# Optimization experiments

Hardware: AMD Instinct MI355X
Metric: run time of the kernel (lower is better)

Reference implementation:

```python
import jax, jax.numpy as jnp
import numpy as np

T, B = 200, 4096
CONTEXT_FRAMES = 6


def _lstm_cell(x, h, c, wih, whh, bih, bhh):
    # PyTorch LSTM gate order: i, f, g, o
    g = x @ wih.T + bih + h @ whh.T + bhh
    i, f, gg, o = jnp.split(g, 4, axis=-1)
    c2 = jax.nn.sigmoid(f) * c + jax.nn.sigmoid(i) * jnp.tanh(gg)
    h2 = jax.nn.sigmoid(o) * jnp.tanh(c2)
    return h2, c2


def _ff(x, w1, b1, w2, b2):
    return jax.nn.relu(jax.nn.relu(x @ w1.T + b1) @ w2.T + b2)


def setup_inputs() -> dict:
    key = jax.random.key(0)
    ks = iter(jax.random.split(key, 48))

    def p(shape, scale=0.1):
        return (jax.random.normal(next(ks), shape) * scale).astype(jnp.float32)

    inp = {
        'tactiles': p((T, B, 48), 1.0),
        'actions': p((T, B, 3), 1.0),
        'context': p((T, B, 48), 1.0),
    }
    # LSTM params: (4H, in), (4H, H), (4H,), (4H,)
    for name, din, h in [('l1', 48, 48), ('l2', 96, 96), ('l3', 144, 144), ('l4', 48, 48)]:
        inp[name + '_wih'] = p((4 * h, din))
        inp[name + '_whh'] = p((4 * h, h))
        inp[name + '_bih'] = p((4 * h,))
        inp[name + '_bhh'] = p((4 * h,))
    # Feedforward params
    for name, din, hid, dout in [('f1', 6, 48, 48), ('f2', 144, 144, 96), ('f3', 96, 96, 48)]:
        inp[name + '_w1'] = p((hid, din))
        inp[name + '_b1'] = p((hid,))
        inp[name + '_w2'] = p((dout, hid))
        inp[name + '_b2'] = p((dout,))
    # Hidden-state inits (original uses torch.rand -> uniform[0,1))
    for name, h in [('1', 48), ('2', 96), ('3', 144), ('4', 48)]:
        inp['h0_' + name] = jax.random.uniform(next(ks), (B, h), dtype=jnp.float32)
        inp['c0_' + name] = jax.random.uniform(next(ks), (B, h), dtype=jnp.float32)
    return inp


def reference(tactiles, actions, context,
              l1_wih, l1_whh, l1_bih, l1_bhh,
              l2_wih, l2_whh, l2_bih, l2_bhh,
              l3_wih, l3_whh, l3_bih, l3_bhh,
              l4_wih, l4_whh, l4_bih, l4_bhh,
              f1_w1, f1_b1, f1_w2, f1_b2,
              f2_w1, f2_b1, f2_w2, f2_b2,
              f3_w1, f3_b1, f3_w2, f3_b2,
              h0_1, c0_1, h0_2, c0_2, h0_3, c0_3, h0_4, c0_4):
    state = actions[0]  # [B, 3], fixed across time

    def step(carry, inp):
        h1, c1, h2, c2, h3, c3, h4, c4, out6 = carry
        tac, act, ctx, t = inp
        x1 = jnp.where(t > CONTEXT_FRAMES - 1, out6, tac)  # [B, 48]
        h1, c1 = _lstm_cell(x1, h1, c1, l1_wih, l1_whh, l1_bih, l1_bhh)
        x2 = jnp.concatenate([ctx, h1], axis=1)  # [B, 96]
        h2, c2 = _lstm_cell(x2, h2, c2, l2_wih, l2_whh, l2_bih, l2_bhh)
        sa = jnp.concatenate([state, act], axis=1)  # [B, 6]
        sa_out = _ff(sa, f1_w1, f1_b1, f1_w2, f1_b2)  # [B, 48]
        x3 = jnp.concatenate([sa_out, h2], axis=1)  # [B, 144]
        h3, c3 = _lstm_cell(x3, h3, c3, l3_wih, l3_whh, l3_bih, l3_bhh)
        out4 = _ff(h3, f2_w1, f2_b1, f2_w2, f2_b2)  # [B, 96]
        out5 = _ff(out4, f3_w1, f3_b1, f3_w2, f3_b2)  # [B, 48]
        h4, c4 = _lstm_cell(out5, h4, c4, l4_wih, l4_whh, l4_bih, l4_bhh)
        return (h1, c1, h2, c2, h3, c3, h4, c4, h4), h4

    carry0 = (h0_1, c0_1, h0_2, c0_2, h0_3, c0_3, h0_4, c0_4, jnp.zeros_like(h0_1))
    ts = jnp.arange(tactiles.shape[0])
    _, outs = jax.lax.scan(step, carry0, (tactiles, actions, context, ts))
    return outs  # [T, B, 48]
```

## Files before the change

kernel.cpp:

```cpp
#include <hip/hip_runtime.h>
#include <math.h>


#define NT 256
#define MROWS 16
#define TSTEPS 200
#define BATCH 4096
#define XS 18
#define GS 17
#define GS8 9

#define L1W   0
#define L1B   18432
#define L2W   18624
#define L2B   92352
#define L3W   92736
#define L3B   258624
#define L4W   259200
#define L4B   277632
#define F1AW  277824
#define F1AB  278208
#define F1BW  278256
#define F1BB  280560
#define F2AW  280608
#define F2AB  301344
#define F2BW  301488
#define F2BB  315312
#define F3AW  315408
#define F3AB  324624
#define F3BW  324720
#define F3BB  329328

#define P_SAT  0
#define P_F1H  144
#define P_GB   0
#define P_F2H  0
#define P_O4T  2592
#define P_F3H  4320
#define P_OUT5 0
#define P_L4G  864
#define POOLSZ 6528

__device__ __forceinline__ float sigf(float x) { return 1.0f / (1.0f + __expf(-x)); }

__global__ void prep_lstm(const float* __restrict__ wih, const float* __restrict__ whh,
                          const float* __restrict__ bih, const float* __restrict__ bhh,
                          float* __restrict__ W, float* __restrict__ bias,
                          int Din, int H) {
    int K = Din + H;
    int N = 4 * H;
    int total = N * K;
    for (int idx = blockIdx.x * blockDim.x + threadIdx.x; idx < total + N;
         idx += gridDim.x * blockDim.x) {
        if (idx < total) {
            int c = idx / K;
            int k = idx - c * K;
            W[idx] = (k < Din) ? wih[c * Din + k] : whh[c * H + (k - Din)];
        } else {
            int c = idx - total;
            bias[c] = bih[c] + bhh[c];
        }
    }
}

__global__ void prep_ff(const float* __restrict__ w, const float* __restrict__ b,
                        float* __restrict__ W, float* __restrict__ bias,
                        int K, int Kpad, int N) {
    int total = N * Kpad;
    for (int idx = blockIdx.x * blockDim.x + threadIdx.x; idx < total + N;
         idx += gridDim.x * blockDim.x) {
        if (idx < total) {
            int c = idx / Kpad;
            int k = idx - c * Kpad;
            W[idx] = (k < K) ? w[c * K + k] : 0.0f;
        } else {
            int c = idx - total;
            bias[c] = b[c];
        }
    }
}

template <int TC, int ROWS, bool RELU>
__device__ __forceinline__ void mm(
    const float* __restrict__ w0, const float* __restrict__ w1,
    const float* __restrict__ w2,
    float b0, float b1, float b2,
    const float* __restrict__ x0, int K0,
    const float* __restrict__ x1, int K1,
    const float* __restrict__ x2, int K2,
    int rbase,
    float* __restrict__ g0, float* __restrict__ g1, float* __restrict__ g2) {
    float a0[ROWS], a1[ROWS], a2[ROWS];
#pragma unroll
    for (int r = 0; r < ROWS; ++r) { a0[r] = 0.f; a1[r] = 0.f; a2[r] = 0.f; }
    int ko = 0;
#pragma unroll
    for (int s = 0; s < 3; ++s) {
        const float* xb = (s == 0) ? x0 : (s == 1) ? x1 : x2;
        int K = (s == 0) ? K0 : (s == 1) ? K1 : K2;
        if (K > 0) {
            const float* xp = xb + rbase;
#pragma unroll 2
            for (int k = 0; k < K; k += 4) {
                float4 wv0 = *(const float4*)(w0 + ko + k);
                float4 wv1 = (TC > 1) ? *(const float4*)(w1 + ko + k) : wv0;
                float4 wv2 = (TC > 2) ? *(const float4*)(w2 + ko + k) : wv0;
                const float* f0 = (const float*)&wv0;
                const float* f1p = (const float*)&wv1;
                const float* f2p = (const float*)&wv2;
#pragma unroll
                for (int q = 0; q < 4; ++q) {
                    const float* xq = xp + (k + q) * XS;
#pragma unroll
                    for (int rr = 0; rr < ROWS; rr += 2) {
                        float2 xv = *(const float2*)(xq + rr);
                        a0[rr]     = fmaf(xv.x, f0[q], a0[rr]);
                        a0[rr + 1] = fmaf(xv.y, f0[q], a0[rr + 1]);
                        if (TC > 1) {
                            a1[rr]     = fmaf(xv.x, f1p[q], a1[rr]);
                            a1[rr + 1] = fmaf(xv.y, f1p[q], a1[rr + 1]);
                        }
                        if (TC > 2) {
                            a2[rr]     = fmaf(xv.x, f2p[q], a2[rr]);
                            a2[rr + 1] = fmaf(xv.y, f2p[q], a2[rr + 1]);
                        }
                    }
                }
            }
            ko += K;
        }
    }
#pragma unroll
    for (int r = 0; r < ROWS; ++r) {
        float v0 = a0[r] + b0;
        if (RELU) v0 = fmaxf(v0, 0.f);
        g0[r] = v0;
        if (TC > 1) {
            float v1 = a1[r] + b1;
            if (RELU) v1 = fmaxf(v1, 0.f);
            g1[r] = v1;
        }
        if (TC > 2) {
            float v2 = a2[r] + b2;
            if (RELU) v2 = fmaxf(v2, 0.f);
            g2[r] = v2;
        }
    }
}

template <int H, int R, int NCS>
__device__ __forceinline__ void lstm_epi(const float* __restrict__ gb, int gs,
                                         float* __restrict__ hT, int hrbase,
                                         float (&cs)[NCS], int tid) {
    const int E = H * R;
#pragma unroll
    for (int n = 0; n < NCS; ++n) {
        int idx = tid + n * NT;
        if (idx < E) {
            int r = idx & (R - 1);
            int j = idx / R;
            float gi = gb[j * gs + r];
            float gf = gb[(j + H) * gs + r];
            float gg = gb[(j + 2 * H) * gs + r];
            float go = gb[(j + 3 * H) * gs + r];
            float c2 = sigf(gf) * cs[n] + sigf(gi) * tanhf(gg);
            cs[n] = c2;
            hT[j * XS + hrbase + r] = sigf(go) * tanhf(c2);
        }
    }
}

template <int H, int R, int NCS>
__device__ __forceinline__ void c_init(const float* __restrict__ c0, int r0,
                                       int rbase, float (&cs)[NCS], int tid) {
    const int E = H * R;
#pragma unroll
    for (int n = 0; n < NCS; ++n) {
        int idx = tid + n * NT;
        if (idx < E) {
            int r = idx & (R - 1);
            int j = idx / R;
            cs[n] = c0[(size_t)(r0 + rbase + r) * H + j];
        }
    }
}

__global__ __launch_bounds__(256, 1) void model_kernel(
    const float* __restrict__ tactiles, const float* __restrict__ actions,
    const float* __restrict__ context, const float* __restrict__ ws,
    const float* __restrict__ h01, const float* __restrict__ c01,
    const float* __restrict__ h02, const float* __restrict__ c02,
    const float* __restrict__ h03, const float* __restrict__ c03,
    const float* __restrict__ h04, const float* __restrict__ c04,
    float* __restrict__ out) {
    __shared__ __align__(16) float tacT[48 * XS];
    __shared__ __align__(16) float ctxT[48 * XS];
    __shared__ __align__(16) float h1T[48 * XS];
    __shared__ __align__(16) float h2T[96 * XS];
    __shared__ __align__(16) float h3T[144 * XS];
    __shared__ __align__(16) float h4T[48 * XS];
    __shared__ __align__(16) float saoT[48 * XS];
    __shared__ __align__(16) float pool[POOLSZ];

    const int tid = threadIdx.x;
    const int r0 = blockIdx.x * MROWS;

    for (int i = tid; i < 48 * 16; i += NT) {
        int r = i & 15, j = i >> 4;
        h1T[j * XS + r] = h01[(size_t)(r0 + r) * 48 + j];
        h4T[j * XS + r] = h04[(size_t)(r0 + r) * 48 + j];
    }
    for (int i = tid; i < 96 * 16; i += NT) {
        int r = i & 15, j = i >> 4;
        h2T[j * XS + r] = h02[(size_t)(r0 + r) * 96 + j];
    }
    for (int i = tid; i < 144 * 16; i += NT) {
        int r = i & 15, j = i >> 4;
        h3T[j * XS + r] = h03[(size_t)(r0 + r) * 144 + j];
    }

    float cs1[3], cs2[6], cs3a[5], cs3b[5], cs4[3];
    c_init<48, 16, 3>(c01, r0, 0, cs1, tid);
    c_init<96, 16, 6>(c02, r0, 0, cs2, tid);
    c_init<144, 8, 5>(c03, r0, 0, cs3a, tid);
    c_init<144, 8, 5>(c03, r0, 8, cs3b, tid);
    c_init<48, 16, 3>(c04, r0, 0, cs4, tid);

    float bL1  = (tid < 192) ? ws[L1B + tid] : 0.f;
    float bL2a = ws[L2B + tid];
    float bL2b = (tid < 128) ? ws[L2B + tid + 256] : 0.f;
    float bL3a = ws[L3B + tid];
    float bL3b = ws[L3B + tid + 256];
    float bL3c = (tid < 64) ? ws[L3B + tid + 512] : 0.f;
    float bL4  = (tid < 192) ? ws[L4B + tid] : 0.f;
    float bF1a = (tid < 48) ? ws[F1AB + tid] : 0.f;
    float bF1b = (tid < 48) ? ws[F1BB + tid] : 0.f;
    float bF2a = (tid < 144) ? ws[F2AB + tid] : 0.f;
    float bF2b = (tid < 192) ? ws[F2BB + (tid % 96)] : 0.f;
    float bF3a = (tid < 192) ? ws[F3AB + (tid % 96)] : 0.f;
    float bF3b = (tid < 192) ? ws[F3BB + (tid % 48)] : 0.f;

    const int wvid = tid >> 6;
    __syncthreads();

    for (int t = 0; t < TSTEPS; ++t) {
        if (t < 6) {
            const float* src = tactiles + (size_t)t * BATCH * 48 + (size_t)r0 * 48;
            for (int i = tid; i < 192; i += NT) {
                int r = i / 12, k4 = (i % 12) * 4;
                float4 v = *(const float4*)(src + r * 48 + k4);
                tacT[(k4 + 0) * XS + r] = v.x;
                tacT[(k4 + 1) * XS + r] = v.y;
                tacT[(k4 + 2) * XS + r] = v.z;
                tacT[(k4 + 3) * XS + r] = v.w;
            }
        }
        {
            const float* src = context + (size_t)t * BATCH * 48 + (size_t)r0 * 48;
            for (int i = tid; i < 192; i += NT) {
                int r = i / 12, k4 = (i % 12) * 4;
                float4 v = *(const float4*)(src + r * 48 + k4);
                ctxT[(k4 + 0) * XS + r] = v.x;
                ctxT[(k4 + 1) * XS + r] = v.y;
                ctxT[(k4 + 2) * XS + r] = v.z;
                ctxT[(k4 + 3) * XS + r] = v.w;
            }
        }
        if (tid < 128) {
            int r = tid & 15, k = tid >> 4;
            float v = 0.f;
            if (k < 3) v = actions[(size_t)(r0 + r) * 3 + k];
            else if (k < 6) v = actions[(size_t)t * BATCH * 3 + (size_t)(r0 + r) * 3 + (k - 3)];
            pool[P_SAT + k * XS + r] = v;
        }
        __syncthreads();

        if (tid < 48)
            mm<1, 16, true>(ws + F1AW + tid * 8, ws, ws, bF1a, 0.f, 0.f,
                            pool + P_SAT, 8, nullptr, 0, nullptr, 0, 0,
                            pool + P_F1H + tid * XS, nullptr, nullptr);
        __syncthreads();
        if (tid < 48)
            mm<1, 16, true>(ws + F1BW + tid * 48, ws, ws, bF1b, 0.f, 0.f,
                            pool + P_F1H, 48, nullptr, 0, nullptr, 0, 0,
                            saoT + tid * XS, nullptr, nullptr);
        __syncthreads();

        {
            const float* x1 = (t < 6) ? tacT : h4T;
            if (tid < 192)
                mm<1, 16, false>(ws + L1W + tid * 96, ws, ws, bL1, 0.f, 0.f,
                                 x1, 48, h1T, 48, nullptr, 0, 0,
                                 pool + P_GB + tid * GS, nullptr, nullptr);
        }
        __syncthreads();
        lstm_epi<48, 16, 3>(pool + P_GB, GS, h1T, 0, cs1, tid);
        __syncthreads();

        if (wvid < 2)
            mm<2, 16, false>(ws + L2W + (size_t)tid * 192, ws + L2W + (size_t)(tid + 256) * 192,
                             ws, bL2a, bL2b, 0.f,
                             ctxT, 48, h1T, 48, h2T, 96, 0,
                             pool + P_GB + tid * GS, pool + P_GB + (tid + 256) * GS, nullptr);
        else
            mm<1, 16, false>(ws + L2W + (size_t)tid * 192, ws, ws, bL2a, 0.f, 0.f,
                             ctxT, 48, h1T, 48, h2T, 96, 0,
                             pool + P_GB + tid * GS, nullptr, nullptr);
        __syncthreads();
        lstm_epi<96, 16, 6>(pool + P_GB, GS, h2T, 0, cs2, tid);
        __syncthreads();

        if (wvid == 0)
            mm<3, 8, false>(ws + L3W + (size_t)tid * 288, ws + L3W + (size_t)(tid + 256) * 288,
                            ws + L3W + (size_t)(tid + 512) * 288, bL3a, bL3b, bL3c,
                            saoT, 48, h2T, 96, h3T, 144, 0,
                            pool + P_GB + tid * GS8, pool + P_GB + (tid + 256) * GS8,
                            pool + P_GB + (tid + 512) * GS8);
        else
            mm<2, 8, false>(ws + L3W + (size_t)tid * 288, ws + L3W + (size_t)(tid + 256) * 288,
                            ws, bL3a, bL3b, 0.f,
                            saoT, 48, h2T, 96, h3T, 144, 0,
                            pool + P_GB + tid * GS8, pool + P_GB + (tid + 256) * GS8, nullptr);
        __syncthreads();
        lstm_epi<144, 8, 5>(pool + P_GB, GS8, h3T, 0, cs3a, tid);
        __syncthreads();
        if (wvid == 0)
            mm<3, 8, false>(ws + L3W + (size_t)tid * 288, ws + L3W + (size_t)(tid + 256) * 288,
                            ws + L3W + (size_t)(tid + 512) * 288, bL3a, bL3b, bL3c,
                            saoT, 48, h2T, 96, h3T, 144, 8,
                            pool + P_GB + tid * GS8, pool + P_GB + (tid + 256) * GS8,
                            pool + P_GB + (tid + 512) * GS8);
        else
            mm<2, 8, false>(ws + L3W + (size_t)tid * 288, ws + L3W + (size_t)(tid + 256) * 288,
                            ws, bL3a, bL3b, 0.f,
                            saoT, 48, h2T, 96, h3T, 144, 8,
                            pool + P_GB + tid * GS8, pool + P_GB + (tid + 256) * GS8, nullptr);
        __syncthreads();
        lstm_epi<144, 8, 5>(pool + P_GB, GS8, h3T, 8, cs3b, tid);
        __syncthreads();

        if (tid < 144)
            mm<1, 16, true>(ws + F2AW + tid * 144, ws, ws, bF2a, 0.f, 0.f,
                            h3T, 144, nullptr, 0, nullptr, 0, 0,
                            pool + P_F2H + tid * XS, nullptr, nullptr);
        __syncthreads();
        if (tid < 192) {
            int c = tid % 96, rb = (tid / 96) * 8;
            mm<1, 8, true>(ws + F2BW + c * 144, ws, ws, bF2b, 0.f, 0.f,
                           pool + P_F2H, 144, nullptr, 0, nullptr, 0, rb,
                           pool + P_O4T + c * XS + rb, nullptr, nullptr);
        }
        __syncthreads();
        if (tid < 192) {
            int c = tid % 96, rb = (tid / 96) * 8;
            mm<1, 8, true>(ws + F3AW + c * 96, ws, ws, bF3a, 0.f, 0.f,
                           pool + P_O4T, 96, nullptr, 0, nullptr, 0, rb,
                           pool + P_F3H + c * XS + rb, nullptr, nullptr);
        }
        __syncthreads();
        if (tid < 192) {
            int c = tid % 48, rb = (tid / 48) * 4;
            mm<1, 4, true>(ws + F3BW + c * 96, ws, ws, bF3b, 0.f, 0.f,
                           pool + P_F3H, 96, nullptr, 0, nullptr, 0, rb,
                           pool + P_OUT5 + c * XS + rb, nullptr, nullptr);
        }
        __syncthreads();

        if (tid < 192)
            mm<1, 16, false>(ws + L4W + tid * 96, ws, ws, bL4, 0.f, 0.f,
                             pool + P_OUT5, 48, h4T, 48, nullptr, 0, 0,
                             pool + P_L4G + tid * GS, nullptr, nullptr);
        __syncthreads();
        lstm_epi<48, 16, 3>(pool + P_L4G, GS, h4T, 0, cs4, tid);
        __syncthreads();

        {
            float* dst = out + (size_t)t * BATCH * 48 + (size_t)r0 * 48;
            for (int i = tid; i < 192; i += NT) {
                int r = i / 12, j4 = (i % 12) * 4;
                float4 v;
                v.x = h4T[(j4 + 0) * XS + r];
                v.y = h4T[(j4 + 1) * XS + r];
                v.z = h4T[(j4 + 2) * XS + r];
                v.w = h4T[(j4 + 3) * XS + r];
                *(float4*)(dst + r * 48 + j4) = v;
            }
        }
        __syncthreads();
    }
}

extern "C" void kernel_launch(void* const* d_in, const int* in_sizes, int n_in,
                              void* d_out, int out_size, void* d_ws, size_t ws_size,
                              hipStream_t stream) {
    const float* tac = (const float*)d_in[0];
    const float* act = (const float*)d_in[1];
    const float* ctx = (const float*)d_in[2];

    const float* l1_wih = (const float*)d_in[3];
    const float* l1_whh = (const float*)d_in[4];
    const float* l1_bih = (const float*)d_in[5];
    const float* l1_bhh = (const float*)d_in[6];
    const float* l2_wih = (const float*)d_in[7];
    const float* l2_whh = (const float*)d_in[8];
    const float* l2_bih = (const float*)d_in[9];
    const float* l2_bhh = (const float*)d_in[10];
    const float* l3_wih = (const float*)d_in[11];
    const float* l3_whh = (const float*)d_in[12];
    const float* l3_bih = (const float*)d_in[13];
    const float* l3_bhh = (const float*)d_in[14];
    const float* l4_wih = (const float*)d_in[15];
    const float* l4_whh = (const float*)d_in[16];
    const float* l4_bih = (const float*)d_in[17];
    const float* l4_bhh = (const float*)d_in[18];

    const float* f1_w1 = (const float*)d_in[19];
    const float* f1_b1 = (const float*)d_in[20];
    const float* f1_w2 = (const float*)d_in[21];
    const float* f1_b2 = (const float*)d_in[22];
    const float* f2_w1 = (const float*)d_in[23];
    const float* f2_b1 = (const float*)d_in[24];
    const float* f2_w2 = (const float*)d_in[25];
    const float* f2_b2 = (const float*)d_in[26];
    const float* f3_w1 = (const float*)d_in[27];
    const float* f3_b1 = (const float*)d_in[28];
    const float* f3_w2 = (const float*)d_in[29];
    const float* f3_b2 = (const float*)d_in[30];

    const float* h01 = (const float*)d_in[31];
    const float* c01 = (const float*)d_in[32];
    const float* h02 = (const float*)d_in[33];
    const float* c02 = (const float*)d_in[34];
    const float* h03 = (const float*)d_in[35];
    const float* c03 = (const float*)d_in[36];
    const float* h04 = (const float*)d_in[37];
    const float* c04 = (const float*)d_in[38];

    float* ws = (float*)d_ws;
    float* out = (float*)d_out;

    dim3 blk(NT);
    hipLaunchKernelGGL(prep_lstm, dim3(96), blk, 0, stream,
                       l1_wih, l1_whh, l1_bih, l1_bhh, ws + L1W, ws + L1B, 48, 48);
    hipLaunchKernelGGL(prep_lstm, dim3(256), blk, 0, stream,
                       l2_wih, l2_whh, l2_bih, l2_bhh, ws + L2W, ws + L2B, 96, 96);
    hipLaunchKernelGGL(prep_lstm, dim3(256), blk, 0, stream,
                       l3_wih, l3_whh, l3_bih, l3_bhh, ws + L3W, ws + L3B, 144, 144);
    hipLaunchKernelGGL(prep_lstm, dim3(96), blk, 0, stream,
                       l4_wih, l4_whh, l4_bih, l4_bhh, ws + L4W, ws + L4B, 48, 48);

    hipLaunchKernelGGL(prep_ff, dim3(4), blk, 0, stream,
                       f1_w1, f1_b1, ws + F1AW, ws + F1AB, 6, 8, 48);
    hipLaunchKernelGGL(prep_ff, dim3(16), blk, 0, stream,
                       f1_w2, f1_b2, ws + F1BW, ws + F1BB, 48, 48, 48);
    hipLaunchKernelGGL(prep_ff, dim3(96), blk, 0, stream,
                       f2_w1, f2_b1, ws + F2AW, ws + F2AB, 144, 144, 144);
    hipLaunchKernelGGL(prep_ff, dim3(64), blk, 0, stream,
                       f2_w2, f2_b2, ws + F2BW, ws + F2BB, 144, 144, 96);
    hipLaunchKernelGGL(prep_ff, dim3(48), blk, 0, stream,
                       f3_w1, f3_b1, ws + F3AW, ws + F3AB, 96, 96, 96);
    hipLaunchKernelGGL(prep_ff, dim3(24), blk, 0, stream,
                       f3_w2, f3_b2, ws + F3BW, ws + F3BB, 96, 96, 48);

    hipLaunchKernelGGL(model_kernel, dim3(BATCH / MROWS), blk, 0, stream,
                       tac, act, ctx, ws,
                       h01, c01, h02, c02, h03, c03, h04, c04, out);
}
```

Measured before the change: 20.11 ms.

## Halve rows per block, run two blocks per CU, overlap FF1 with LSTM1

```diff
diff --git a/kernel.cpp b/kernel.cpp
--- a/kernel.cpp
+++ b/kernel.cpp
@@ -3,12 +3,11 @@
 
 
 #define NT 256
-#define MROWS 16
+#define MROWS 8
 #define TSTEPS 200
 #define BATCH 4096
-#define XS 18
-#define GS 17
-#define GS8 9
+#define XS 10
+#define GS 9
 
 #define L1W   0
 #define L1B   18432
@@ -31,15 +30,15 @@
 #define F3BW  324720
 #define F3BB  329328
 
-#define P_SAT  0
-#define P_F1H  144
 #define P_GB   0
+#define P_SAT  5184
+#define P_F1H  5264
 #define P_F2H  0
-#define P_O4T  2592
-#define P_F3H  4320
-#define P_OUT5 0
-#define P_L4G  864
-#define POOLSZ 6528
+#define P_O4T  1440
+#define P_F3H  2400
+#define P_OUT5 3360
+#define P_L4G  0
+#define POOLSZ 5744
 
 __device__ __forceinline__ float sigf(float x) { return 1.0f / (1.0f + __expf(-x)); }
 
@@ -150,12 +149,12 @@
 
 template <int H, int R, int NCS>
 __device__ __forceinline__ void lstm_epi(const float* __restrict__ gb, int gs,
-                                         float* __restrict__ hT, int hrbase,
-                                         float (&cs)[NCS], int tid) {
+                                         float* __restrict__ hT,
+                                         float (&cs)[NCS], int idx0, int stride) {
     const int E = H * R;
 #pragma unroll
     for (int n = 0; n < NCS; ++n) {
-        int idx = tid + n * NT;
+        int idx = idx0 + n * stride;
         if (idx < E) {
             int r = idx & (R - 1);
             int j = idx / R;
@@ -165,27 +164,27 @@
             float go = gb[(j + 3 * H) * gs + r];
             float c2 = sigf(gf) * cs[n] + sigf(gi) * tanhf(gg);
             cs[n] = c2;
-            hT[j * XS + hrbase + r] = sigf(go) * tanhf(c2);
+            hT[j * XS + r] = sigf(go) * tanhf(c2);
         }
     }
 }
 
 template <int H, int R, int NCS>
 __device__ __forceinline__ void c_init(const float* __restrict__ c0, int r0,
-                                       int rbase, float (&cs)[NCS], int tid) {
+                                       float (&cs)[NCS], int idx0, int stride) {
     const int E = H * R;
 #pragma unroll
     for (int n = 0; n < NCS; ++n) {
-        int idx = tid + n * NT;
+        int idx = idx0 + n * stride;
         if (idx < E) {
             int r = idx & (R - 1);
             int j = idx / R;
-            cs[n] = c0[(size_t)(r0 + rbase + r) * H + j];
-        }
-    }
-}
-
-__global__ __launch_bounds__(256, 1) void model_kernel(
+            cs[n] = c0[(size_t)(r0 + r) * H + j];
+        }
+    }
+}
+
+__global__ __launch_bounds__(256, 2) void model_kernel(
     const float* __restrict__ tactiles, const float* __restrict__ actions,
     const float* __restrict__ context, const float* __restrict__ ws,
     const float* __restrict__ h01, const float* __restrict__ c01,
@@ -205,26 +204,28 @@
     const int tid = threadIdx.x;
     const int r0 = blockIdx.x * MROWS;
 
-    for (int i = tid; i < 48 * 16; i += NT) {
-        int r = i & 15, j = i >> 4;
+    for (int i = tid; i < 48 * 8; i += NT) {
+        int r = i & 7, j = i >> 3;
         h1T[j * XS + r] = h01[(size_t)(r0 + r) * 48 + j];
         h4T[j * XS + r] = h04[(size_t)(r0 + r) * 48 + j];
     }
-    for (int i = tid; i < 96 * 16; i += NT) {
-        int r = i & 15, j = i >> 4;
+    for (int i = tid; i < 96 * 8; i += NT) {
+        int r = i & 7, j = i >> 3;
         h2T[j * XS + r] = h02[(size_t)(r0 + r) * 96 + j];
     }
-    for (int i = tid; i < 144 * 16; i += NT) {
-        int r = i & 15, j = i >> 4;
+    for (int i = tid; i < 144 * 8; i += NT) {
+        int r = i & 7, j = i >> 3;
         h3T[j * XS + r] = h03[(size_t)(r0 + r) * 144 + j];
     }
 
-    float cs1[3], cs2[6], cs3a[5], cs3b[5], cs4[3];
-    c_init<48, 16, 3>(c01, r0, 0, cs1, tid);
-    c_init<96, 16, 6>(c02, r0, 0, cs2, tid);
-    c_init<144, 8, 5>(c03, r0, 0, cs3a, tid);
-    c_init<144, 8, 5>(c03, r0, 8, cs3b, tid);
-    c_init<48, 16, 3>(c04, r0, 0, cs4, tid);
+    float cs1[2] = {0.f, 0.f};
+    float cs2[3] = {0.f, 0.f, 0.f};
+    float cs3[5] = {0.f, 0.f, 0.f, 0.f, 0.f};
+    float cs4[2] = {0.f, 0.f};
+    if (tid >= 64) c_init<48, 8, 2>(c01, r0, cs1, tid - 64, 192);
+    c_init<96, 8, 3>(c02, r0, cs2, tid, NT);
+    c_init<144, 8, 5>(c03, r0, cs3, tid, NT);
+    c_init<48, 8, 2>(c04, r0, cs4, tid, NT);
 
     float bL1  = (tid < 192) ? ws[L1B + tid] : 0.f;
     float bL2a = ws[L2B + tid];
@@ -233,7 +234,7 @@
     float bL3b = ws[L3B + tid + 256];
     float bL3c = (tid < 64) ? ws[L3B + tid + 512] : 0.f;
     float bL4  = (tid < 192) ? ws[L4B + tid] : 0.f;
-    float bF1a = (tid < 48) ? ws[F1AB + tid] : 0.f;
+    float bF1a = (tid >= 192 && tid < 240) ? ws[F1AB + (tid - 192)] : 0.f;
     float bF1b = (tid < 48) ? ws[F1BB + tid] : 0.f;
     float bF2a = (tid < 144) ? ws[F2AB + tid] : 0.f;
     float bF2b = (tid < 192) ? ws[F2BB + (tid % 96)] : 0.f;
@@ -246,7 +247,7 @@
     for (int t = 0; t < TSTEPS; ++t) {
         if (t < 6) {
             const float* src = tactiles + (size_t)t * BATCH * 48 + (size_t)r0 * 48;
-            for (int i = tid; i < 192; i += NT) {
+            for (int i = tid; i < 96; i += NT) {
                 int r = i / 12, k4 = (i % 12) * 4;
                 float4 v = *(const float4*)(src + r * 48 + k4);
                 tacT[(k4 + 0) * XS + r] = v.x;
@@ -257,7 +258,7 @@
         }
         {
             const float* src = context + (size_t)t * BATCH * 48 + (size_t)r0 * 48;
-            for (int i = tid; i < 192; i += NT) {
+            for (int i = tid; i < 96; i += NT) {
                 int r = i / 12, k4 = (i % 12) * 4;
                 float4 v = *(const float4*)(src + r * 48 + k4);
                 ctxT[(k4 + 0) * XS + r] = v.x;
@@ -266,8 +267,8 @@
                 ctxT[(k4 + 3) * XS + r] = v.w;
             }
         }
-        if (tid < 128) {
-            int r = tid & 15, k = tid >> 4;
+        if (tid < 64) {
+            int r = tid & 7, k = tid >> 3;
             float v = 0.f;
             if (k < 3) v = actions[(size_t)(r0 + r) * 3 + k];
             else if (k < 6) v = actions[(size_t)t * BATCH * 3 + (size_t)(r0 + r) * 3 + (k - 3)];
@@ -275,108 +276,93 @@
         }
         __syncthreads();
 
-        if (tid < 48)
-            mm<1, 16, true>(ws + F1AW + tid * 8, ws, ws, bF1a, 0.f, 0.f,
-                            pool + P_SAT, 8, nullptr, 0, nullptr, 0, 0,
-                            pool + P_F1H + tid * XS, nullptr, nullptr);
-        __syncthreads();
-        if (tid < 48)
-            mm<1, 16, true>(ws + F1BW + tid * 48, ws, ws, bF1b, 0.f, 0.f,
-                            pool + P_F1H, 48, nullptr, 0, nullptr, 0, 0,
-                            saoT + tid * XS, nullptr, nullptr);
-        __syncthreads();
-
         {
             const float* x1 = (t < 6) ? tacT : h4T;
             if (tid < 192)
-                mm<1, 16, false>(ws + L1W + tid * 96, ws, ws, bL1, 0.f, 0.f,
-                                 x1, 48, h1T, 48, nullptr, 0, 0,
-                                 pool + P_GB + tid * GS, nullptr, nullptr);
-        }
-        __syncthreads();
-        lstm_epi<48, 16, 3>(pool + P_GB, GS, h1T, 0, cs1, tid);
+                mm<1, 8, false>(ws + L1W + tid * 96, ws, ws, bL1, 0.f, 0.f,
+                                x1, 48, h1T, 48, nullptr, 0, 0,
+                                pool + P_GB + tid * GS, nullptr, nullptr);
+            else if (tid < 240)
+                mm<1, 8, true>(ws + F1AW + (tid - 192) * 8, ws, ws, bF1a, 0.f, 0.f,
+                               pool + P_SAT, 8, nullptr, 0, nullptr, 0, 0,
+                               pool + P_F1H + (tid - 192) * XS, nullptr, nullptr);
+        }
+        __syncthreads();
+
+        if (tid < 48)
+            mm<1, 8, true>(ws + F1BW + tid * 48, ws, ws, bF1b, 0.f, 0.f,
+                           pool + P_F1H, 48, nullptr, 0, nullptr, 0, 0,
+                           saoT + tid * XS, nullptr, nullptr);
+        else if (tid >= 64)
+            lstm_epi<48, 8, 2>(pool + P_GB, GS, h1T, cs1, tid - 64, 192);
         __syncthreads();
 
         if (wvid < 2)
-            mm<2, 16, false>(ws + L2W + (size_t)tid * 192, ws + L2W + (size_t)(tid + 256) * 192,
-                             ws, bL2a, bL2b, 0.f,
-                             ctxT, 48, h1T, 48, h2T, 96, 0,
-                             pool + P_GB + tid * GS, pool + P_GB + (tid + 256) * GS, nullptr);
+            mm<2, 8, false>(ws + L2W + (size_t)tid * 192, ws + L2W + (size_t)(tid + 256) * 192,
+                            ws, bL2a, bL2b, 0.f,
+                            ctxT, 48, h1T, 48, h2T, 96, 0,
+                            pool + P_GB + tid * GS, pool + P_GB + (tid + 256) * GS, nullptr);
         else
-            mm<1, 16, false>(ws + L2W + (size_t)tid * 192, ws, ws, bL2a, 0.f, 0.f,
-                             ctxT, 48, h1T, 48, h2T, 96, 0,
-                             pool + P_GB + tid * GS, nullptr, nullptr);
-        __syncthreads();
-        lstm_epi<96, 16, 6>(pool + P_GB, GS, h2T, 0, cs2, tid);
+            mm<1, 8, false>(ws + L2W + (size_t)tid * 192, ws, ws, bL2a, 0.f, 0.f,
+                            ctxT, 48, h1T, 48, h2T, 96, 0,
+                            pool + P_GB + tid * GS, nullptr, nullptr);
+        __syncthreads();
+        lstm_epi<96, 8, 3>(pool + P_GB, GS, h2T, cs2, tid, NT);
         __syncthreads();
 
         if (wvid == 0)
             mm<3, 8, false>(ws + L3W + (size_t)tid * 288, ws + L3W + (size_t)(tid + 256) * 288,
                             ws + L3W + (size_t)(tid + 512) * 288, bL3a, bL3b, bL3c,
                             saoT, 48, h2T, 96, h3T, 144, 0,
-                            pool + P_GB + tid * GS8, pool + P_GB + (tid + 256) * GS8,
-                            pool + P_GB + (tid + 512) * GS8);
+                            pool + P_GB + tid * GS, pool + P_GB + (tid + 256) * GS,
+                            pool + P_GB + (tid + 512) * GS);
         else
             mm<2, 8, false>(ws + L3W + (size_t)tid * 288, ws + L3W + (size_t)(tid + 256) * 288,
                             ws, bL3a, bL3b, 0.f,
                             saoT, 48, h2T, 96, h3T, 144, 0,
-                            pool + P_GB + tid * GS8, pool + P_GB + (tid + 256) * GS8, nullptr);
-        __syncthreads();
-        lstm_epi<144, 8, 5>(pool + P_GB, GS8, h3T, 0, cs3a, tid);
-        __syncthreads();
-        if (wvid == 0)
-            mm<3, 8, false>(ws + L3W + (size_t)tid * 288, ws + L3W + (size_t)(tid + 256) * 288,
-                            ws + L3W + (size_t)(tid + 512) * 288, bL3a, bL3b, bL3c,
-                            saoT, 48, h2T, 96, h3T, 144, 8,
-                            pool + P_GB + tid * GS8, pool + P_GB + (tid + 256) * GS8,
-                            pool + P_GB + (tid + 512) * GS8);
-        else
-            mm<2, 8, false>(ws + L3W + (size_t)tid * 288, ws + L3W + (size_t)(tid + 256) * 288,
-                            ws, bL3a, bL3b, 0.f,
-                            saoT, 48, h2T, 96, h3T, 144, 8,
-                            pool + P_GB + tid * GS8, pool + P_GB + (tid + 256) * GS8, nullptr);
-        __syncthreads();
-        lstm_epi<144, 8, 5>(pool + P_GB, GS8, h3T, 8, cs3b, tid);
+                            pool + P_GB + tid * GS, pool + P_GB + (tid + 256) * GS, nullptr);
+        __syncthreads();
+        lstm_epi<144, 8, 5>(pool + P_GB, GS, h3T, cs3, tid, NT);
         __syncthreads();
 
         if (tid < 144)
-            mm<1, 16, true>(ws + F2AW + tid * 144, ws, ws, bF2a, 0.f, 0.f,
-                            h3T, 144, nullptr, 0, nullptr, 0, 0,
-                            pool + P_F2H + tid * XS, nullptr, nullptr);
+            mm<1, 8, true>(ws + F2AW + tid * 144, ws, ws, bF2a, 0.f, 0.f,
+                           h3T, 144, nullptr, 0, nullptr, 0, 0,
+                           pool + P_F2H + tid * XS, nullptr, nullptr);
         __syncthreads();
         if (tid < 192) {
-            int c = tid % 96, rb = (tid / 96) * 8;
-            mm<1, 8, true>(ws + F2BW + c * 144, ws, ws, bF2b, 0.f, 0.f,
+            int c = tid % 96, rb = (tid / 96) * 4;
+            mm<1, 4, true>(ws + F2BW + c * 144, ws, ws, bF2b, 0.f, 0.f,
                            pool + P_F2H, 144, nullptr, 0, nullptr, 0, rb,
                            pool + P_O4T + c * XS + rb, nullptr, nullptr);
         }
         __syncthreads();
         if (tid < 192) {
-            int c = tid % 96, rb = (tid / 96) * 8;
-            mm<1, 8, true>(ws + F3AW + c * 96, ws, ws, bF3a, 0.f, 0.f,
+            int c = tid % 96, rb = (tid / 96) * 4;
+            mm<1, 4, true>(ws + F3AW + c * 96, ws, ws, bF3a, 0.f, 0.f,
                            pool + P_O4T, 96, nullptr, 0, nullptr, 0, rb,
                            pool + P_F3H + c * XS + rb, nullptr, nullptr);
         }
         __syncthreads();
         if (tid < 192) {
-            int c = tid % 48, rb = (tid / 48) * 4;
-            mm<1, 4, true>(ws + F3BW + c * 96, ws, ws, bF3b, 0.f, 0.f,
+            int c = tid % 48, rb = (tid / 48) * 2;
+            mm<1, 2, true>(ws + F3BW + c * 96, ws, ws, bF3b, 0.f, 0.f,
                            pool + P_F3H, 96, nullptr, 0, nullptr, 0, rb,
                            pool + P_OUT5 + c * XS + rb, nullptr, nullptr);
         }
         __syncthreads();
 
         if (tid < 192)
-            mm<1, 16, false>(ws + L4W + tid * 96, ws, ws, bL4, 0.f, 0.f,
-                             pool + P_OUT5, 48, h4T, 48, nullptr, 0, 0,
-                             pool + P_L4G + tid * GS, nullptr, nullptr);
-        __syncthreads();
-        lstm_epi<48, 16, 3>(pool + P_L4G, GS, h4T, 0, cs4, tid);
+            mm<1, 8, false>(ws + L4W + tid * 96, ws, ws, bL4, 0.f, 0.f,
+                            pool + P_OUT5, 48, h4T, 48, nullptr, 0, 0,
+                            pool + P_L4G + tid * GS, nullptr, nullptr);
+        __syncthreads();
+        lstm_epi<48, 8, 2>(pool + P_L4G, GS, h4T, cs4, tid, NT);
         __syncthreads();
 
         {
             float* dst = out + (size_t)t * BATCH * 48 + (size_t)r0 * 48;
-            for (int i = tid; i < 192; i += NT) {
+            for (int i = tid; i < 96; i += NT) {
                 int r = i / 12, j4 = (i % 12) * 4;
                 float4 v;
                 v.x = h4T[(j4 + 0) * XS + r];
@@ -386,7 +372,6 @@
                 *(float4*)(dst + r * 48 + j4) = v;
             }
         }
-        __syncthreads();
     }
 }
 
```

Result: faster. 17.68 ms (-12.1%).
